# Performance work log

Hardware: AMD Instinct MI355X
Metric: run time of the kernel (lower is better)

The kernel has to match this reference:

```python
import jax, jax.numpy as jnp
import numpy as np

N_NODES = 50000
N_EDGES = 1000000
N_GRAPHS = 64
IN_FEATS, HIDDEN, N_CLASSES = 64, 64, 32


def setup_inputs() -> dict:
    key = jax.random.key(0)
    ks = jax.random.split(key, 10)
    x = jax.random.normal(ks[0], (N_NODES, IN_FEATS), dtype=jnp.float32)
    eh = jax.random.normal(ks[1], (N_EDGES,), dtype=jnp.float32)
    src = jax.random.randint(ks[2], (N_EDGES,), 0, N_NODES)
    dst = jax.random.randint(ks[3], (N_EDGES,), 0, N_NODES)
    node_graph = jnp.sort(jax.random.randint(ks[4], (N_NODES,), 0, N_GRAPHS))
    # GraphConv parameters (glorot-ish scale)
    W1 = jax.random.normal(ks[5], (IN_FEATS, HIDDEN), dtype=jnp.float32) / np.sqrt(IN_FEATS)
    b1 = jnp.zeros((HIDDEN,), dtype=jnp.float32)
    W2 = jax.random.normal(ks[6], (HIDDEN, N_CLASSES), dtype=jnp.float32) / np.sqrt(HIDDEN)
    b2 = jnp.zeros((N_CLASSES,), dtype=jnp.float32)
    mu = jnp.array(0.0, dtype=jnp.float32)
    # sigma = -1.0 keeps log((eh-mu)^2 / -sigma) in a valid domain (module default 1.0 -> NaN)
    sigma = jnp.array(-1.0, dtype=jnp.float32)
    return {"x": x, "eh": eh, "src": src, "dst": dst, "node_graph": node_graph,
            "W1": W1, "b1": b1, "W2": W2, "b2": b2, "mu": mu, "sigma": sigma}


def _graph_conv(x, W, b, src, dst, ew, norm_src, norm_dst):
    # DGL GraphConv(norm='both') with per-edge scalar weight ew:
    # h = D_in^{-1/2} * A_w * (D_out^{-1/2} * x) @ W + b
    xs = x * norm_src  # [N, F]
    msg = xs[src] * ew[:, None]  # gather + edge-weight multiply  [E, F]
    agg = jax.ops.segment_sum(msg, dst, num_segments=x.shape[0])  # scatter-add [N, F]
    return (agg * norm_dst) @ W + b


def reference(x, eh, src, dst, node_graph, W1, b1, W2, b2, mu, sigma):
    n = x.shape[0]
    ones_e = jnp.ones_like(eh)
    deg_out = jnp.clip(jax.ops.segment_sum(ones_e, src, num_segments=n), 1.0)
    deg_in = jnp.clip(jax.ops.segment_sum(ones_e, dst, num_segments=n), 1.0)
    norm_src = jax.lax.rsqrt(deg_out)[:, None]  # [N,1]
    norm_dst = jax.lax.rsqrt(deg_in)[:, None]   # [N,1]

    # edge feature transform: log((h - mu)^2 / -sigma)
    d = eh - mu
    efeat = jnp.log(d * d / -sigma)  # [E]

    h = _graph_conv(x, W1, b1, src, dst, efeat, norm_src, norm_dst)
    h = jax.nn.relu(h)
    h = _graph_conv(h, W2, b2, src, dst, efeat, norm_src, norm_dst)

    # dgl.mean_nodes: per-graph mean over nodes
    g_sum = jax.ops.segment_sum(h, node_graph, num_segments=N_GRAPHS)  # [B, C]
    g_cnt = jnp.clip(jax.ops.segment_sum(jnp.ones((n,), jnp.float32), node_graph,
                                         num_segments=N_GRAPHS), 1.0)
    return g_sum / g_cnt[:, None]
```

## Files before the change

kernel.cpp:

```cpp
#include <hip/hip_runtime.h>

#define NGRAPHS 64
#define NCLS 32
#define G1 256

__device__ inline unsigned bfpack(float lo, float hi) {
    unsigned ulo = __float_as_uint(lo); ulo += 0x7fffu + ((ulo >> 16) & 1u);
    unsigned uhi = __float_as_uint(hi); uhi += 0x7fffu + ((uhi >> 16) & 1u);
    return (ulo >> 16) | (uhi & 0xffff0000u);
}
__device__ inline float bflo(unsigned p) { return __uint_as_float(p << 16); }
__device__ inline float bfhi(unsigned p) { return __uint_as_float(p & 0xffff0000u); }
__device__ inline float bfs(unsigned short u) { return __uint_as_float((unsigned)u << 16); }

__global__ __launch_bounds__(256) void part_hist(const int* __restrict__ src,
    const int* __restrict__ dst, int* __restrict__ gHd, int* __restrict__ gHs,
    int* __restrict__ gLocD, int* __restrict__ gLocS, int nE) {
    __shared__ int hd[256], hs[256], tmp[256];
    int t = threadIdx.x, blk = blockIdx.x;
    hd[t] = 0; hs[t] = 0;
    __syncthreads();
    int chunk = (nE + G1 - 1) / G1;
    int beg = blk * chunk, end = min(beg + chunk, nE);
    for (int i = beg + t; i < end; i += 256) {
        atomicAdd(&hd[((unsigned)dst[i]) >> 8], 1);
        atomicAdd(&hs[((unsigned)src[i]) >> 8], 1);
    }
    __syncthreads();
    gHd[t * G1 + blk] = hd[t];
    gHs[t * G1 + blk] = hs[t];
    tmp[t] = hd[t];
    __syncthreads();
    for (int o = 1; o < 256; o <<= 1) {
        int u = (t >= o) ? tmp[t - o] : 0;
        __syncthreads();
        tmp[t] += u;
        __syncthreads();
    }
    gLocD[blk * 256 + t] = tmp[t] - hd[t];
    __syncthreads();
    tmp[t] = hs[t];
    __syncthreads();
    for (int o = 1; o < 256; o <<= 1) {
        int u = (t >= o) ? tmp[t - o] : 0;
        __syncthreads();
        tmp[t] += u;
        __syncthreads();
    }
    gLocS[blk * 256 + t] = tmp[t] - hs[t];
}

__global__ __launch_bounds__(1024) void part_scan(int* __restrict__ a, int* __restrict__ b) {
    __shared__ int part[1024];
    int* arr = blockIdx.x ? b : a;
    int t = threadIdx.x;
    int base = t * 64;
    int v[64], s = 0;
#pragma unroll
    for (int j = 0; j < 64; ++j) { v[j] = arr[base + j]; s += v[j]; }
    part[t] = s;
    __syncthreads();
    for (int o = 1; o < 1024; o <<= 1) {
        int u = (t >= o) ? part[t - o] : 0;
        __syncthreads();
        part[t] += u;
        __syncthreads();
    }
    int run = part[t] - s;
#pragma unroll
    for (int j = 0; j < 64; ++j) { arr[base + j] = run; run += v[j]; }
    if (t == 1023) arr[65536] = run;
}

__global__ __launch_bounds__(256) void part_scatter(const float* __restrict__ eh,
    const int* __restrict__ src, const int* __restrict__ dst,
    const float* __restrict__ mu, const float* __restrict__ sigma,
    const int* __restrict__ gLocD, const int* __restrict__ gLocS,
    int2* __restrict__ partD, unsigned char* __restrict__ partS, int nE) {
    __shared__ int hd[256], hs[256], locD[256], locS[256];
    int t = threadIdx.x, blk = blockIdx.x;
    hd[t] = 0; hs[t] = 0;
    locD[t] = gLocD[blk * 256 + t];
    locS[t] = gLocS[blk * 256 + t];
    __syncthreads();
    float mu0 = mu[0], inv = -1.f / sigma[0];
    int chunk = (nE + G1 - 1) / G1;
    size_t wbase = (size_t)blk * chunk;
    int beg = blk * chunk, end = min(beg + chunk, nE);
    for (int i = beg + t; i < end; i += 256) {
        int d = dst[i], s = src[i];
        float df = eh[i] - mu0;
        float w = logf(df * df * inv);
        int bu = ((unsigned)d) >> 8;
        int r = atomicAdd(&hd[bu], 1);
        partD[wbase + locD[bu] + r] = make_int2((s << 8) | (d & 255), __float_as_int(w));
        int bs = ((unsigned)s) >> 8;
        int r2 = atomicAdd(&hs[bs], 1);
        partS[wbase + locS[bs] + r2] = (unsigned char)(s & 255);
    }
}

__global__ __launch_bounds__(256) void bucket_build(const int2* __restrict__ partD,
    const unsigned char* __restrict__ partS, const int* __restrict__ gHd,
    const int* __restrict__ gHs, const int* __restrict__ gLocD,
    const int* __restrict__ gLocS, int* __restrict__ csr_src,
    unsigned short* __restrict__ csr_w, int* __restrict__ row_start,
    float* __restrict__ norm_dst, float* __restrict__ norm_src, int nN, int nE) {
    __shared__ int deg[256], loff[256], cnt[256];
    int b = blockIdx.x, t = threadIdx.x;
    int chunk = (nE + G1 - 1) / G1;
    int begD = gHd[b * G1];
    int lenD = gHd[b * G1 + t + 1] - gHd[b * G1 + t];
    size_t offD = (size_t)t * chunk + gLocD[t * 256 + b];
    deg[t] = 0; cnt[t] = 0;
    __syncthreads();
    for (int i = 0; i < lenD; ++i)
        atomicAdd(&deg[partD[offD + i].x & 255], 1);
    __syncthreads();
    loff[t] = deg[t];
    __syncthreads();
    for (int o = 1; o < 256; o <<= 1) {
        int u = (t >= o) ? loff[t - o] : 0;
        __syncthreads();
        loff[t] += u;
        __syncthreads();
    }
    loff[t] -= deg[t];
    __syncthreads();
    int n = b * 256 + t;
    if (n < nN) {
        row_start[n] = begD + loff[t];
        norm_dst[n] = rsqrtf((float)max(deg[t], 1));
    }
    if (b == 0 && t == 0) row_start[nN] = nE;
    for (int i = 0; i < lenD; ++i) {
        int2 r = partD[offD + i];
        int lo = r.x & 255;
        int pos = atomicAdd(&cnt[lo], 1);
        int idx = begD + loff[lo] + pos;
        csr_src[idx] = r.x >> 8;
        unsigned uw = (unsigned)r.y;
        csr_w[idx] = (unsigned short)((uw + 0x7fffu + ((uw >> 16) & 1u)) >> 16);
    }
    __syncthreads();
    deg[t] = 0;
    __syncthreads();
    int lenS = gHs[b * G1 + t + 1] - gHs[b * G1 + t];
    size_t offS = (size_t)t * chunk + gLocS[t * 256 + b];
    for (int i = 0; i < lenS; ++i)
        atomicAdd(&deg[partS[offS + i]], 1);
    __syncthreads();
    if (n < nN) norm_src[n] = rsqrtf((float)max(deg[t], 1));
}

__global__ __launch_bounds__(256) void xw_mm(const float* __restrict__ x,
    const float* __restrict__ norm_src, const float* __restrict__ W1,
    unsigned* __restrict__ xw, int nN) {
    __shared__ float sW[64 * 64];
    __shared__ float srow[4][64];
    int t = threadIdx.x;
    for (int i = t; i < 64 * 64; i += 256) sW[i] = W1[i];
    __syncthreads();
    int wid = t >> 6, k = t & 63;
    int base = blockIdx.x * 32;
    for (int it = 0; it < 8; ++it) {
        int n = base + it * 4 + wid;
        if (n >= nN) break;
        srow[wid][k] = x[((size_t)n << 6) + k] * norm_src[n];
        float acc0 = 0.f, acc1 = 0.f;
#pragma unroll
        for (int i = 0; i < 64; i += 2) {
            acc0 += srow[wid][i] * sW[i * 64 + k];
            acc1 += srow[wid][i + 1] * sW[(i + 1) * 64 + k];
        }
        float outv = acc0 + acc1;
        float other = __shfl_xor(outv, 1, 64);
        if ((k & 1) == 0) xw[((size_t)n << 5) + (k >> 1)] = bfpack(outv, other);
    }
}

__global__ __launch_bounds__(256) void gather1_mm(const unsigned* __restrict__ xw,
    const int* __restrict__ row_start, const int* __restrict__ csr_src,
    const unsigned short* __restrict__ csr_w, const float* __restrict__ norm_dst,
    const float* __restrict__ norm_src, const float* __restrict__ W2f,
    const float* __restrict__ b1, unsigned* __restrict__ hw, int nN) {
    __shared__ float sW[64 * NCLS];
    __shared__ float srow[4][64];
    __shared__ int rs[17];
    int t = threadIdx.x;
    int base = blockIdx.x * 16;
    for (int i = t; i < 64 * NCLS; i += 256) sW[i] = W2f[i];
    if (t < 17) rs[t] = row_start[min(base + t, nN)];
    __syncthreads();
    int wid = t >> 6, lane = t & 63;
    int q = lane >> 4, j = lane & 15;
    const uint2* xw2 = reinterpret_cast<const uint2*>(xw);
    float4 bv = reinterpret_cast<const float4*>(b1)[j];
    for (int it = 0; it < 4; ++it) {
        int n = base + it * 4 + wid;
        if (n >= nN) break;
        int beg = __builtin_amdgcn_readfirstlane(rs[it * 4 + wid]);
        int end = __builtin_amdgcn_readfirstlane(rs[it * 4 + wid + 1]);
        float a0 = 0.f, a1 = 0.f, a2 = 0.f, a3 = 0.f;
        for (int sl0 = beg + q; sl0 < end; sl0 += 24) {
            int s[6]; float w[6];
#pragma unroll
            for (int u = 0; u < 6; ++u) {
                int sl = sl0 + 4 * u;
                int slc = (sl < end) ? sl : (end - 1);
                s[u] = csr_src[slc];
                float wv = bfs(csr_w[slc]);
                w[u] = (sl < end) ? wv : 0.f;
            }
            uint2 p[6];
#pragma unroll
            for (int u = 0; u < 6; ++u) p[u] = xw2[((size_t)s[u] << 4) + j];
#pragma unroll
            for (int u = 0; u < 6; ++u) {
                a0 += w[u] * bflo(p[u].x); a1 += w[u] * bfhi(p[u].x);
                a2 += w[u] * bflo(p[u].y); a3 += w[u] * bfhi(p[u].y);
            }
        }
        a0 += __shfl_xor(a0, 16, 64); a0 += __shfl_xor(a0, 32, 64);
        a1 += __shfl_xor(a1, 16, 64); a1 += __shfl_xor(a1, 32, 64);
        a2 += __shfl_xor(a2, 16, 64); a2 += __shfl_xor(a2, 32, 64);
        a3 += __shfl_xor(a3, 16, 64); a3 += __shfl_xor(a3, 32, 64);
        float nd = norm_dst[n], ns = norm_src[n];
        if (q == 0) {
            float4 v;
            v.x = fmaxf(a0 * nd + bv.x, 0.f) * ns;
            v.y = fmaxf(a1 * nd + bv.y, 0.f) * ns;
            v.z = fmaxf(a2 * nd + bv.z, 0.f) * ns;
            v.w = fmaxf(a3 * nd + bv.w, 0.f) * ns;
            *reinterpret_cast<float4*>(&srow[wid][4 * j]) = v;
        }
        int jj = lane & 31, ib = lane & 32;
        float acc0 = 0.f, acc1 = 0.f;
#pragma unroll
        for (int i = 0; i < 32; i += 2) {
            acc0 += srow[wid][ib + i] * sW[(ib + i) * NCLS + jj];
            acc1 += srow[wid][ib + i + 1] * sW[(ib + i + 1) * NCLS + jj];
        }
        float part = acc0 + acc1;
        part += __shfl_xor(part, 32, 64);
        float other = __shfl_xor(part, 1, 64);
        if (ib == 0 && (jj & 1) == 0)
            hw[((size_t)n << 4) + (jj >> 1)] = bfpack(part, other);
    }
}

__global__ __launch_bounds__(256) void gather2(const unsigned* __restrict__ hw,
    const int* __restrict__ row_start, const int* __restrict__ csr_src,
    const unsigned short* __restrict__ csr_w, const float* __restrict__ norm_dst,
    unsigned* __restrict__ agg2, int nN) {
    __shared__ int rs[17];
    int t = threadIdx.x;
    int base = blockIdx.x * 16;
    if (t < 17) rs[t] = row_start[min(base + t, nN)];
    __syncthreads();
    int wid = t >> 6, lane = t & 63;
    int o = lane >> 3, j = lane & 7;
    const uint2* hw2 = reinterpret_cast<const uint2*>(hw);
    for (int it = 0; it < 4; ++it) {
        int n = base + it * 4 + wid;
        if (n >= nN) break;
        int beg = __builtin_amdgcn_readfirstlane(rs[it * 4 + wid]);
        int end = __builtin_amdgcn_readfirstlane(rs[it * 4 + wid + 1]);
        float a0 = 0.f, a1 = 0.f, a2 = 0.f, a3 = 0.f;
        for (int sl0 = beg + o; sl0 < end; sl0 += 16) {
            int s[2]; float w[2];
#pragma unroll
            for (int u = 0; u < 2; ++u) {
                int sl = sl0 + 8 * u;
                int slc = (sl < end) ? sl : (end - 1);
                s[u] = csr_src[slc];
                float wv = bfs(csr_w[slc]);
                w[u] = (sl < end) ? wv : 0.f;
            }
            uint2 p[2];
#pragma unroll
            for (int u = 0; u < 2; ++u) p[u] = hw2[((size_t)s[u] << 3) + j];
#pragma unroll
            for (int u = 0; u < 2; ++u) {
                a0 += w[u] * bflo(p[u].x); a1 += w[u] * bfhi(p[u].x);
                a2 += w[u] * bflo(p[u].y); a3 += w[u] * bfhi(p[u].y);
            }
        }
        a0 += __shfl_xor(a0, 8, 64); a0 += __shfl_xor(a0, 16, 64); a0 += __shfl_xor(a0, 32, 64);
        a1 += __shfl_xor(a1, 8, 64); a1 += __shfl_xor(a1, 16, 64); a1 += __shfl_xor(a1, 32, 64);
        a2 += __shfl_xor(a2, 8, 64); a2 += __shfl_xor(a2, 16, 64); a2 += __shfl_xor(a2, 32, 64);
        a3 += __shfl_xor(a3, 8, 64); a3 += __shfl_xor(a3, 16, 64); a3 += __shfl_xor(a3, 32, 64);
        if (lane < 8) {
            float nd = norm_dst[n];
            uint2 out;
            out.x = bfpack(a0 * nd, a1 * nd);
            out.y = bfpack(a2 * nd, a3 * nd);
            reinterpret_cast<uint2*>(agg2)[((size_t)n << 3) + j] = out;
        }
    }
}

__global__ __launch_bounds__(256) void pool_out(const unsigned* __restrict__ agg2,
    const int* __restrict__ ng, const float* __restrict__ b2,
    float* __restrict__ out, int nN) {
    __shared__ float gacc[NCLS];
    int g = blockIdx.x, t = threadIdx.x;
    if (t < NCLS) gacc[t] = 0.f;
    __syncthreads();
    int lo = 0, hi = nN;
    while (lo < hi) { int m = (lo + hi) >> 1; if (ng[m] < g) lo = m + 1; else hi = m; }
    int lb = lo;
    lo = 0; hi = nN;
    while (lo < hi) { int m = (lo + hi) >> 1; if (ng[m] < g + 1) lo = m + 1; else hi = m; }
    int ub = lo;
    int r = t >> 4, j = t & 15;
    float ax = 0.f, ay = 0.f;
    for (int n = lb + r; n < ub; n += 16) {
        unsigned p = agg2[((size_t)n << 4) + j];
        ax += bflo(p); ay += bfhi(p);
    }
    atomicAdd(&gacc[2 * j], ax);
    atomicAdd(&gacc[2 * j + 1], ay);
    __syncthreads();
    if (t < NCLS) {
        float cnt = (float)(ub - lb);
        out[g * NCLS + t] = (gacc[t] + b2[t] * cnt) / fmaxf(cnt, 1.f);
    }
}

extern "C" void kernel_launch(void* const* d_in, const int* in_sizes, int n_in,
                              void* d_out, int out_size, void* d_ws, size_t ws_size,
                              hipStream_t stream) {
    const float* x   = (const float*)d_in[0];
    const float* eh  = (const float*)d_in[1];
    const int*   src = (const int*)d_in[2];
    const int*   dst = (const int*)d_in[3];
    const int*   ng  = (const int*)d_in[4];
    const float* W1  = (const float*)d_in[5];
    const float* b1  = (const float*)d_in[6];
    const float* W2  = (const float*)d_in[7];
    const float* b2  = (const float*)d_in[8];
    const float* mu  = (const float*)d_in[9];
    const float* sg  = (const float*)d_in[10];
    const int nN = in_sizes[0] / 64;
    const int nE = in_sizes[1];
    const int NBUK = (nN + 255) / 256;
    const int chunk = (nE + G1 - 1) / G1;

    char* wsb = (char*)d_ws;
    int* gHd = (int*)wsb;
    int* gHs = gHd + 65537;
    int* gLocD = gHs + 65537;
    int* gLocS = gLocD + 65536;
    int* row_start = gLocS + 65536;
    float* norm_src = (float*)(row_start + nN + 1);
    float* norm_dst = norm_src + nN;
    size_t off = (size_t)((char*)(norm_dst + nN) - wsb);
    off = (off + 15) & ~(size_t)15;
    int2* partD = (int2*)(wsb + off);
    unsigned char* partS = (unsigned char*)(partD + (size_t)G1 * chunk);
    off = (size_t)((char*)(partS + (size_t)G1 * chunk) - wsb);
    off = (off + 15) & ~(size_t)15;
    int* csr_src = (int*)(wsb + off);
    unsigned short* csr_w = (unsigned short*)(csr_src + nE);
    off = (size_t)((char*)(csr_w + nE) - wsb);
    off = (off + 15) & ~(size_t)15;
    unsigned* xw   = (unsigned*)(wsb + off);
    unsigned* hw   = xw + (size_t)nN * 32;
    unsigned* agg2 = hw + (size_t)nN * 16;

    part_hist<<<G1, 256, 0, stream>>>(src, dst, gHd, gHs, gLocD, gLocS, nE);
    part_scan<<<2, 1024, 0, stream>>>(gHd, gHs);
    part_scatter<<<G1, 256, 0, stream>>>(eh, src, dst, mu, sg, gLocD, gLocS,
                                         partD, partS, nE);
    bucket_build<<<NBUK, 256, 0, stream>>>(partD, partS, gHd, gHs, gLocD, gLocS,
                                           csr_src, csr_w, row_start,
                                           norm_dst, norm_src, nN, nE);
    xw_mm<<<(nN + 31) / 32, 256, 0, stream>>>(x, norm_src, W1, xw, nN);
    gather1_mm<<<(nN + 15) / 16, 256, 0, stream>>>(xw, row_start, csr_src, csr_w,
                                                   norm_dst, norm_src, W2, b1, hw, nN);
    gather2<<<(nN + 15) / 16, 256, 0, stream>>>(hw, row_start, csr_src, csr_w,
                                                norm_dst, agg2, nN);
    pool_out<<<NGRAPHS, 256, 0, stream>>>(agg2, ng, b2, (float*)d_out, nN);

    (void)n_in; (void)out_size; (void)ws_size;
}
```

Baseline: 180.3 us.

## Software-pipeline node gathers across rows in gather kernels with double buffers

Replaces the per-node loop in gather1_mm and gather2 with a manually unrolled schedule over the four nodes each wave handles. Two register buffers (A and B) let the CSR index loads and feature gathers for the next node(s) be issued before the current node's accumulation and epilogue run, hiding gather latency. Out-of-range nodes are handled by clamped indices and guarded stores instead of an early break. Costs more registers, which may lower occupancy, and adds much more code through macros.

Measured after the change: 169.6 us. -5.9%, faster.

```diff
diff --git a/kernel.cpp b/kernel.cpp
--- a/kernel.cpp
+++ b/kernel.cpp
@@ -179,6 +179,61 @@
     }
 }
 
+#define LCSR(P, bg, en) { \
+    int last_ = max((en) - 1, 0); \
+    _Pragma("unroll") \
+    for (int u = 0; u < 6; ++u) { \
+        int sl = (bg) + q + 4 * u; \
+        int slc = (sl < (en)) ? sl : last_; \
+        P##s[u] = csr_src[slc]; \
+        float wv = bfs(csr_w[slc]); \
+        P##w[u] = (sl < (en)) ? wv : 0.f; \
+    } }
+#define LGAT(P) { \
+    _Pragma("unroll") \
+    for (int u = 0; u < 6; ++u) P##p[u] = xw2[((size_t)P##s[u] << 4) + j]; }
+#define LFMA(P) { \
+    _Pragma("unroll") \
+    for (int u = 0; u < 6; ++u) { \
+        a0 += P##w[u] * bflo(P##p[u].x); a1 += P##w[u] * bfhi(P##p[u].x); \
+        a2 += P##w[u] * bflo(P##p[u].y); a3 += P##w[u] * bfhi(P##p[u].y); } }
+#define REM(P, bg, en) { \
+    for (int sl0 = (bg) + q + 24; sl0 < (en); sl0 += 24) { \
+        int last_ = (en) - 1; \
+        _Pragma("unroll") \
+        for (int u = 0; u < 6; ++u) { \
+            int sl = sl0 + 4 * u; \
+            int slc = (sl < (en)) ? sl : last_; \
+            P##s[u] = csr_src[slc]; \
+            float wv = bfs(csr_w[slc]); \
+            P##w[u] = (sl < (en)) ? wv : 0.f; } \
+        _Pragma("unroll") \
+        for (int u = 0; u < 6; ++u) P##p[u] = xw2[((size_t)P##s[u] << 4) + j]; \
+        LFMA(P) } }
+#define EPI(nd_, ns_, n_) { \
+    a0 += __shfl_xor(a0, 16, 64); a0 += __shfl_xor(a0, 32, 64); \
+    a1 += __shfl_xor(a1, 16, 64); a1 += __shfl_xor(a1, 32, 64); \
+    a2 += __shfl_xor(a2, 16, 64); a2 += __shfl_xor(a2, 32, 64); \
+    a3 += __shfl_xor(a3, 16, 64); a3 += __shfl_xor(a3, 32, 64); \
+    if (q == 0) { \
+        float4 v; \
+        v.x = fmaxf(a0 * (nd_) + bv.x, 0.f) * (ns_); \
+        v.y = fmaxf(a1 * (nd_) + bv.y, 0.f) * (ns_); \
+        v.z = fmaxf(a2 * (nd_) + bv.z, 0.f) * (ns_); \
+        v.w = fmaxf(a3 * (nd_) + bv.w, 0.f) * (ns_); \
+        *reinterpret_cast<float4*>(&srow[wid][4 * j]) = v; } \
+    { int jj = lane & 31, ib = lane & 32; \
+      float c0 = 0.f, c1 = 0.f; \
+      _Pragma("unroll") \
+      for (int i = 0; i < 32; i += 2) { \
+          c0 += srow[wid][ib + i] * sW[(ib + i) * NCLS + jj]; \
+          c1 += srow[wid][ib + i + 1] * sW[(ib + i + 1) * NCLS + jj]; } \
+      float part = c0 + c1; \
+      part += __shfl_xor(part, 32, 64); \
+      float other = __shfl_xor(part, 1, 64); \
+      if (ib == 0 && (jj & 1) == 0 && (n_) < nN) \
+          hw[((size_t)(n_) << 4) + (jj >> 1)] = bfpack(part, other); } }
+
 __global__ __launch_bounds__(256) void gather1_mm(const unsigned* __restrict__ xw,
     const int* __restrict__ row_start, const int* __restrict__ csr_src,
     const unsigned short* __restrict__ csr_w, const float* __restrict__ norm_dst,
@@ -196,58 +251,90 @@
     int q = lane >> 4, j = lane & 15;
     const uint2* xw2 = reinterpret_cast<const uint2*>(xw);
     float4 bv = reinterpret_cast<const float4*>(b1)[j];
-    for (int it = 0; it < 4; ++it) {
-        int n = base + it * 4 + wid;
-        if (n >= nN) break;
-        int beg = __builtin_amdgcn_readfirstlane(rs[it * 4 + wid]);
-        int end = __builtin_amdgcn_readfirstlane(rs[it * 4 + wid + 1]);
-        float a0 = 0.f, a1 = 0.f, a2 = 0.f, a3 = 0.f;
-        for (int sl0 = beg + q; sl0 < end; sl0 += 24) {
-            int s[6]; float w[6];
-#pragma unroll
-            for (int u = 0; u < 6; ++u) {
-                int sl = sl0 + 4 * u;
-                int slc = (sl < end) ? sl : (end - 1);
-                s[u] = csr_src[slc];
-                float wv = bfs(csr_w[slc]);
-                w[u] = (sl < end) ? wv : 0.f;
-            }
-            uint2 p[6];
-#pragma unroll
-            for (int u = 0; u < 6; ++u) p[u] = xw2[((size_t)s[u] << 4) + j];
-#pragma unroll
-            for (int u = 0; u < 6; ++u) {
-                a0 += w[u] * bflo(p[u].x); a1 += w[u] * bfhi(p[u].x);
-                a2 += w[u] * bflo(p[u].y); a3 += w[u] * bfhi(p[u].y);
-            }
-        }
-        a0 += __shfl_xor(a0, 16, 64); a0 += __shfl_xor(a0, 32, 64);
-        a1 += __shfl_xor(a1, 16, 64); a1 += __shfl_xor(a1, 32, 64);
-        a2 += __shfl_xor(a2, 16, 64); a2 += __shfl_xor(a2, 32, 64);
-        a3 += __shfl_xor(a3, 16, 64); a3 += __shfl_xor(a3, 32, 64);
-        float nd = norm_dst[n], ns = norm_src[n];
-        if (q == 0) {
-            float4 v;
-            v.x = fmaxf(a0 * nd + bv.x, 0.f) * ns;
-            v.y = fmaxf(a1 * nd + bv.y, 0.f) * ns;
-            v.z = fmaxf(a2 * nd + bv.z, 0.f) * ns;
-            v.w = fmaxf(a3 * nd + bv.w, 0.f) * ns;
-            *reinterpret_cast<float4*>(&srow[wid][4 * j]) = v;
-        }
-        int jj = lane & 31, ib = lane & 32;
-        float acc0 = 0.f, acc1 = 0.f;
-#pragma unroll
-        for (int i = 0; i < 32; i += 2) {
-            acc0 += srow[wid][ib + i] * sW[(ib + i) * NCLS + jj];
-            acc1 += srow[wid][ib + i + 1] * sW[(ib + i + 1) * NCLS + jj];
-        }
-        float part = acc0 + acc1;
-        part += __shfl_xor(part, 32, 64);
-        float other = __shfl_xor(part, 1, 64);
-        if (ib == 0 && (jj & 1) == 0)
-            hw[((size_t)n << 4) + (jj >> 1)] = bfpack(part, other);
-    }
-}
+    int n0 = base + wid, n1 = n0 + 4, n2 = n0 + 8, n3 = n0 + 12;
+    int nc = nN - 1;
+    float nd0 = norm_dst[min(n0, nc)], ns0 = norm_src[min(n0, nc)];
+    float nd1 = norm_dst[min(n1, nc)], ns1 = norm_src[min(n1, nc)];
+    float nd2 = norm_dst[min(n2, nc)], ns2 = norm_src[min(n2, nc)];
+    float nd3 = norm_dst[min(n3, nc)], ns3 = norm_src[min(n3, nc)];
+    int r0b = __builtin_amdgcn_readfirstlane(rs[wid]);
+    int r0e = __builtin_amdgcn_readfirstlane(rs[wid + 1]);
+    int r1b = __builtin_amdgcn_readfirstlane(rs[wid + 4]);
+    int r1e = __builtin_amdgcn_readfirstlane(rs[wid + 5]);
+    int r2b = __builtin_amdgcn_readfirstlane(rs[wid + 8]);
+    int r2e = __builtin_amdgcn_readfirstlane(rs[wid + 9]);
+    int r3b = __builtin_amdgcn_readfirstlane(rs[wid + 12]);
+    int r3e = __builtin_amdgcn_readfirstlane(rs[wid + 13]);
+    int As[6]; float Aw[6]; uint2 Ap[6];
+    int Bs[6]; float Bw[6]; uint2 Bp[6];
+    float a0, a1, a2, a3;
+    LCSR(A, r0b, r0e)
+    LGAT(A)
+    LCSR(B, r1b, r1e)
+    LGAT(B)
+    a0 = a1 = a2 = a3 = 0.f;
+    LFMA(A)
+    REM(A, r0b, r0e)
+    LCSR(A, r2b, r2e)
+    EPI(nd0, ns0, n0)
+    LGAT(A)
+    a0 = a1 = a2 = a3 = 0.f;
+    LFMA(B)
+    REM(B, r1b, r1e)
+    LCSR(B, r3b, r3e)
+    EPI(nd1, ns1, n1)
+    LGAT(B)
+    a0 = a1 = a2 = a3 = 0.f;
+    LFMA(A)
+    REM(A, r2b, r2e)
+    EPI(nd2, ns2, n2)
+    a0 = a1 = a2 = a3 = 0.f;
+    LFMA(B)
+    REM(B, r3b, r3e)
+    EPI(nd3, ns3, n3)
+}
+
+#define LCSR2(P, bg, en) { \
+    int last_ = max((en) - 1, 0); \
+    _Pragma("unroll") \
+    for (int u = 0; u < 2; ++u) { \
+        int sl = (bg) + o + 8 * u; \
+        int slc = (sl < (en)) ? sl : last_; \
+        P##s[u] = csr_src[slc]; \
+        float wv = bfs(csr_w[slc]); \
+        P##w[u] = (sl < (en)) ? wv : 0.f; \
+    } }
+#define LGAT2(P) { \
+    _Pragma("unroll") \
+    for (int u = 0; u < 2; ++u) P##p[u] = hw2[((size_t)P##s[u] << 3) + j]; }
+#define LFMA2(P) { \
+    _Pragma("unroll") \
+    for (int u = 0; u < 2; ++u) { \
+        a0 += P##w[u] * bflo(P##p[u].x); a1 += P##w[u] * bfhi(P##p[u].x); \
+        a2 += P##w[u] * bflo(P##p[u].y); a3 += P##w[u] * bfhi(P##p[u].y); } }
+#define REM2(P, bg, en) { \
+    for (int sl0 = (bg) + o + 16; sl0 < (en); sl0 += 16) { \
+        int last_ = (en) - 1; \
+        _Pragma("unroll") \
+        for (int u = 0; u < 2; ++u) { \
+            int sl = sl0 + 8 * u; \
+            int slc = (sl < (en)) ? sl : last_; \
+            P##s[u] = csr_src[slc]; \
+            float wv = bfs(csr_w[slc]); \
+            P##w[u] = (sl < (en)) ? wv : 0.f; } \
+        _Pragma("unroll") \
+        for (int u = 0; u < 2; ++u) P##p[u] = hw2[((size_t)P##s[u] << 3) + j]; \
+        LFMA2(P) } }
+#define EPI2(nd_, n_) { \
+    a0 += __shfl_xor(a0, 8, 64); a0 += __shfl_xor(a0, 16, 64); a0 += __shfl_xor(a0, 32, 64); \
+    a1 += __shfl_xor(a1, 8, 64); a1 += __shfl_xor(a1, 16, 64); a1 += __shfl_xor(a1, 32, 64); \
+    a2 += __shfl_xor(a2, 8, 64); a2 += __shfl_xor(a2, 16, 64); a2 += __shfl_xor(a2, 32, 64); \
+    a3 += __shfl_xor(a3, 8, 64); a3 += __shfl_xor(a3, 16, 64); a3 += __shfl_xor(a3, 32, 64); \
+    if (lane < 8 && (n_) < nN) { \
+        uint2 outv; \
+        outv.x = bfpack(a0 * (nd_), a1 * (nd_)); \
+        outv.y = bfpack(a2 * (nd_), a3 * (nd_)); \
+        reinterpret_cast<uint2*>(agg2)[((size_t)(n_) << 3) + j] = outv; } }
 
 __global__ __launch_bounds__(256) void gather2(const unsigned* __restrict__ hw,
     const int* __restrict__ row_start, const int* __restrict__ csr_src,
@@ -261,43 +348,45 @@
     int wid = t >> 6, lane = t & 63;
     int o = lane >> 3, j = lane & 7;
     const uint2* hw2 = reinterpret_cast<const uint2*>(hw);
-    for (int it = 0; it < 4; ++it) {
-        int n = base + it * 4 + wid;
-        if (n >= nN) break;
-        int beg = __builtin_amdgcn_readfirstlane(rs[it * 4 + wid]);
-        int end = __builtin_amdgcn_readfirstlane(rs[it * 4 + wid + 1]);
-        float a0 = 0.f, a1 = 0.f, a2 = 0.f, a3 = 0.f;
-        for (int sl0 = beg + o; sl0 < end; sl0 += 16) {
-            int s[2]; float w[2];
-#pragma unroll
-            for (int u = 0; u < 2; ++u) {
-                int sl = sl0 + 8 * u;
-                int slc = (sl < end) ? sl : (end - 1);
-                s[u] = csr_src[slc];
-                float wv = bfs(csr_w[slc]);
-                w[u] = (sl < end) ? wv : 0.f;
-            }
-            uint2 p[2];
-#pragma unroll
-            for (int u = 0; u < 2; ++u) p[u] = hw2[((size_t)s[u] << 3) + j];
-#pragma unroll
-            for (int u = 0; u < 2; ++u) {
-                a0 += w[u] * bflo(p[u].x); a1 += w[u] * bfhi(p[u].x);
-                a2 += w[u] * bflo(p[u].y); a3 += w[u] * bfhi(p[u].y);
-            }
-        }
-        a0 += __shfl_xor(a0, 8, 64); a0 += __shfl_xor(a0, 16, 64); a0 += __shfl_xor(a0, 32, 64);
-        a1 += __shfl_xor(a1, 8, 64); a1 += __shfl_xor(a1, 16, 64); a1 += __shfl_xor(a1, 32, 64);
-        a2 += __shfl_xor(a2, 8, 64); a2 += __shfl_xor(a2, 16, 64); a2 += __shfl_xor(a2, 32, 64);
-        a3 += __shfl_xor(a3, 8, 64); a3 += __shfl_xor(a3, 16, 64); a3 += __shfl_xor(a3, 32, 64);
-        if (lane < 8) {
-            float nd = norm_dst[n];
-            uint2 out;
-            out.x = bfpack(a0 * nd, a1 * nd);
-            out.y = bfpack(a2 * nd, a3 * nd);
-            reinterpret_cast<uint2*>(agg2)[((size_t)n << 3) + j] = out;
-        }
-    }
+    int n0 = base + wid, n1 = n0 + 4, n2 = n0 + 8, n3 = n0 + 12;
+    int nc = nN - 1;
+    float nd0 = norm_dst[min(n0, nc)], nd1 = norm_dst[min(n1, nc)];
+    float nd2 = norm_dst[min(n2, nc)], nd3 = norm_dst[min(n3, nc)];
+    int r0b = __builtin_amdgcn_readfirstlane(rs[wid]);
+    int r0e = __builtin_amdgcn_readfirstlane(rs[wid + 1]);
+    int r1b = __builtin_amdgcn_readfirstlane(rs[wid + 4]);
+    int r1e = __builtin_amdgcn_readfirstlane(rs[wid + 5]);
+    int r2b = __builtin_amdgcn_readfirstlane(rs[wid + 8]);
+    int r2e = __builtin_amdgcn_readfirstlane(rs[wid + 9]);
+    int r3b = __builtin_amdgcn_readfirstlane(rs[wid + 12]);
+    int r3e = __builtin_amdgcn_readfirstlane(rs[wid + 13]);
+    int As[2]; float Aw[2]; uint2 Ap[2];
+    int Bs[2]; float Bw[2]; uint2 Bp[2];
+    float a0, a1, a2, a3;
+    LCSR2(A, r0b, r0e)
+    LGAT2(A)
+    LCSR2(B, r1b, r1e)
+    LGAT2(B)
+    a0 = a1 = a2 = a3 = 0.f;
+    LFMA2(A)
+    REM2(A, r0b, r0e)
+    LCSR2(A, r2b, r2e)
+    EPI2(nd0, n0)
+    LGAT2(A)
+    a0 = a1 = a2 = a3 = 0.f;
+    LFMA2(B)
+    REM2(B, r1b, r1e)
+    LCSR2(B, r3b, r3e)
+    EPI2(nd1, n1)
+    LGAT2(B)
+    a0 = a1 = a2 = a3 = 0.f;
+    LFMA2(A)
+    REM2(A, r2b, r2e)
+    EPI2(nd2, n2)
+    a0 = a1 = a2 = a3 = 0.f;
+    LFMA2(B)
+    REM2(B, r3b, r3e)
+    EPI2(nd3, n3)
 }
 
 __global__ __launch_bounds__(256) void pool_out(const unsigned* __restrict__ agg2,
```
